# Optimization experiments

Measured on AMD Instinct MI355X. Metric: run time of the kernel, lower is better.

The kernel has to match this reference:

```python
import jax, jax.numpy as jnp
import numpy as np

B = 2
T = 32768          # exp.n_samples = 2**15
NB = 128           # exp.n_bands (filter bank bands)
CH = 128           # channels
EC = 512           # encoding_channels
ATOM = 2048        # full_atom_size
FBK = 512          # filter bank kernel size
DILS = (1, 3, 9, 27, 81, 243, 1)


def setup_inputs() -> dict:
    key = jax.random.key(0)
    ks = jax.random.split(key, 8)
    s = 0.05
    return {
        'x': jax.random.normal(ks[0], (B, 1, T), jnp.float32),
        'fb_w': jax.random.normal(ks[1], (NB, 1, FBK), jnp.float32) * s,
        'conv0_w': jax.random.normal(ks[2], (CH, NB, 7), jnp.float32) * s,
        'conv0_b': jnp.zeros((CH,), jnp.float32),
        'bn0_g': jnp.ones((CH,), jnp.float32),
        'bn0_b': jnp.zeros((CH,), jnp.float32),
        'dil_w': jax.random.normal(ks[3], (7, CH, CH, 3), jnp.float32) * s,
        'dil_b': jnp.zeros((7, CH), jnp.float32),
        'pw_w': jax.random.normal(ks[4], (7, CH, CH, 1), jnp.float32) * s,
        'pw_b': jnp.zeros((7, CH), jnp.float32),
        'bn_g': jnp.ones((7, CH), jnp.float32),
        'bn_b': jnp.zeros((7, CH), jnp.float32),
        'up_w': jax.random.normal(ks[5], (EC, CH, 1), jnp.float32) * s,
        'up_b': jnp.zeros((EC,), jnp.float32),
        'static_dict': jax.random.uniform(ks[6], (1, EC, ATOM), jnp.float32, -1.0, 1.0),
    }


def _conv1d(x, w, b=None, dilation=1, padding=0):
    y = jax.lax.conv_general_dilated(
        x, w, (1,), [(padding, padding)], rhs_dilation=(dilation,),
        dimension_numbers=('NCH', 'OIH', 'NCH'))
    if b is not None:
        y = y + b[None, :, None]
    return y


def _bn(x, g, b, eps=1e-5):
    # BatchNorm1d in training mode: per-channel stats over (batch, time)
    m = x.mean(axis=(0, 2), keepdims=True)
    v = x.var(axis=(0, 2), keepdims=True)
    return (x - m) * jax.lax.rsqrt(v + eps) * g[None, :, None] + b[None, :, None]


def _lrelu(x):
    return jnp.where(x >= 0, x, 0.2 * x)


def _fft_convolve(a, b):
    # linear convolution via zero-padded rfft, truncated back to n samples
    n = a.shape[-1]
    fa = jnp.fft.rfft(a, n=2 * n, axis=-1)
    fb = jnp.fft.rfft(b, n=2 * n, axis=-1)
    return jnp.fft.irfft(fa * fb, n=2 * n, axis=-1)[..., :n]


def reference(x, fb_w, conv0_w, conv0_b, bn0_g, bn0_b, dil_w, dil_b,
              pw_w, pw_b, bn_g, bn_b, up_w, up_b, static_dict):
    Bsz, _, n = x.shape
    # filter bank analysis: [B,1,T] -> [B,NB,T]
    spec = _conv1d(x, fb_w, padding=FBK // 2)[..., :n]
    # front conv + leaky relu + BN
    h = _conv1d(spec, conv0_w, conv0_b, padding=3)
    h = _bn(_lrelu(h), bn0_g, bn0_b)
    # dilated residual blocks (dropout = identity at inference)
    for i, d in enumerate(DILS):
        orig = h
        y = _conv1d(h, dil_w[i], dil_b[i], dilation=d, padding=d)
        y = _conv1d(y, pw_w[i], pw_b[i])
        h = _bn(_lrelu(y + orig), bn_g[i], bn_b[i])
    # up-projection to encoding channels + relu
    encoding = jax.nn.relu(_conv1d(h, up_w, up_b))  # [B,EC,T]
    # static dictionary atoms, zero-padded to n_samples, convolved with encoding
    atoms = jnp.broadcast_to(static_dict, (Bsz, EC, ATOM))
    atoms = jnp.pad(atoms, ((0, 0), (0, 0), (0, n - ATOM)))
    final = _fft_convolve(atoms, encoding)          # [B,EC,T]
    return jnp.sum(final, axis=1, keepdims=True)    # [B,1,T]
```

## Files before the change

### kernel.cpp

```cpp
#include <hip/hip_runtime.h>
#include <hip/hip_bf16.h>

#define B_ 2
#define T_ 32768
#define CH_ 128
#define EC_ 512
#define ATOM_ 2048
#define FBK_ 512

typedef __attribute__((ext_vector_type(8))) short s16x8;
typedef __attribute__((ext_vector_type(8))) _Float16 f16x8;
typedef __attribute__((ext_vector_type(4))) float f32x4;

__device__ __forceinline__ f16x8 ldh8(const _Float16* p) {
    union { s16x8 s; f16x8 h; } u; u.s = *(const s16x8*)p; return u.h;
}

__global__ void __launch_bounds__(256) k_fbm(const float* __restrict__ x,
        const _Float16* __restrict__ Wfb, _Float16* __restrict__ spec16) {
    __shared__ _Float16 XA[128][72];
    __shared__ float xw[640];
    int tid = threadIdx.x;
    int lane = tid & 63;
    int wv = tid >> 6, wm = wv >> 1, wn = wv & 1;
    int ln15 = lane & 15, kh = lane >> 4;
    int t0 = blockIdx.x * 128;
    int b = blockIdx.y;

    for (int i = tid; i < 640; i += 256) {
        int g = t0 - 256 + i;
        xw[i] = (g >= 0 && g < T_) ? x[(size_t)b*T_ + g] : 0.f;
    }

    f32x4 acc[4][4];
    f32x4 zero = {0.f,0.f,0.f,0.f};
#pragma unroll
    for (int m = 0; m < 4; ++m)
#pragma unroll
        for (int n = 0; n < 4; ++n) acc[m][n] = zero;

    for (int c = 0; c < 8; ++c) {
        int k0 = c*64;
        __syncthreads();
#pragma unroll
        for (int q = 0; q < 4; ++q) {
            int idx = tid + q*256;
            int r = idx >> 3, ko = idx & 7;
            int base = r + k0 + ko*8;
            f16x8 v;
#pragma unroll
            for (int j = 0; j < 8; ++j) v[j] = (_Float16)xw[base + j];
            union { f16x8 h; s16x8 s; } u; u.h = v;
            *(s16x8*)&XA[r][ko*8] = u.s;
        }
        __syncthreads();
#pragma unroll
        for (int kt = 0; kt < 2; ++kt) {
            f16x8 af[4], bf[4];
#pragma unroll
            for (int m = 0; m < 4; ++m) af[m] = ldh8(&XA[wm*64+m*16+ln15][kt*32+kh*8]);
#pragma unroll
            for (int n = 0; n < 4; ++n)
                bf[n] = ldh8(Wfb + (size_t)(wn*64+n*16+ln15)*FBK_ + k0 + kt*32 + kh*8);
#pragma unroll
            for (int m = 0; m < 4; ++m)
#pragma unroll
                for (int n = 0; n < 4; ++n)
                    acc[m][n] = __builtin_amdgcn_mfma_f32_16x16x32_f16(af[m], bf[n], acc[m][n], 0,0,0);
        }
    }
#pragma unroll
    for (int mf = 0; mf < 4; ++mf)
#pragma unroll
        for (int nf = 0; nf < 4; ++nf) {
            int band = wn*64 + nf*16 + ln15;
#pragma unroll
            for (int j = 0; j < 4; ++j) {
                int tl = wm*64 + mf*16 + kh*4 + j;
                spec16[((size_t)b*T_ + t0 + tl)*CH_ + band] = (_Float16)acc[mf][nf][j];
            }
        }
}

__global__ void k_pw7(const float* __restrict__ w, _Float16* __restrict__ W7) {
    int i = blockIdx.x*256+threadIdx.x;
    if (i >= 7*16384) return;
    int k = i / 16384, r = i % 16384; int co = r >> 7, ci = r & 127;
    W7[i] = (_Float16)w[(co*CH_+ci)*7 + k];
}
__global__ void k_pwd(const float* __restrict__ w, _Float16* __restrict__ Wd) {
    int i = blockIdx.x*256+threadIdx.x;
    if (i >= 7*3*16384) return;
    int st = i / 49152, r = i % 49152; int k = r / 16384, r2 = r % 16384;
    int co = r2 >> 7, ci = r2 & 127;
    Wd[i] = (_Float16)w[((size_t)(st*CH_+co)*CH_+ci)*3 + k];
}
__global__ void k_cast(const float* __restrict__ in, _Float16* __restrict__ out, int n) {
    int i = blockIdx.x*256+threadIdx.x;
    if (i < n) out[i] = (_Float16)in[i];
}
__global__ void k_zero(float* __restrict__ p, int n) {
    int i = blockIdx.x*256+threadIdx.x;
    if (i < n) p[i] = 0.f;
}

template<int NTAP, bool NORM, bool PW, bool LRELU, bool RELU, bool STATS>
__global__ void __launch_bounds__(256) k_cv(
        const _Float16* __restrict__ in, const _Float16* __restrict__ W,
        const float* __restrict__ bias, const _Float16* __restrict__ Wp_,
        const float* __restrict__ pbias, const float* __restrict__ stats_in,
        const float* __restrict__ g, const float* __restrict__ bb,
        float* __restrict__ stats_out, _Float16* __restrict__ outp,
        int dil, int ostride) {
    __shared__ _Float16 XT[128][136];
    __shared__ _Float16 Y1[PW?128:1][PW?136:1];
    __shared__ float AffA[NORM?128:1], AffB[NORM?128:1];

    int tid = threadIdx.x;
    int lane = tid & 63;
    int wv = tid >> 6, wm = wv >> 1, wn = wv & 1;
    int ln15 = lane & 15, kh = lane >> 4;
    int t0 = blockIdx.x * 128;
    int nch = blockIdx.y;
    int b = blockIdx.z;
    int ncol0 = nch * 128;
    const _Float16* inb = in + (size_t)b*T_*CH_;
    const _Float16* W_eff = W + (size_t)ncol0*CH_;
    const float* bias_eff = bias + ncol0;

    if (NORM) {
        if (tid < 128) {
            const float invN = 1.f/(float)(B_*T_);
            float s1 = stats_in[tid], s2 = stats_in[128+tid];
            float m = s1*invN, var = s2*invN - m*m;
            float A = rsqrtf(var + 1e-5f) * g[tid];
            AffA[tid] = A; AffB[tid] = bb[tid] - m*A;
        }
    }

    f32x4 acc[4][4];
    f32x4 zero = {0.f,0.f,0.f,0.f};
#pragma unroll
    for (int m = 0; m < 4; ++m)
#pragma unroll
        for (int n = 0; n < 4; ++n) acc[m][n] = zero;

    for (int tap = 0; tap < NTAP; ++tap) {
        int tp = tap;
        if (PW) tp = (tap==0) ? 0 : ((tap==1) ? 2 : 1);
        int off = (tp - NTAP/2)*dil;
        const _Float16* Wt = W_eff + (size_t)tp*CH_*CH_;
        __syncthreads();
#pragma unroll
        for (int q = 0; q < 8; ++q) {
            int idx = tid + q*256;
            int lt = idx >> 4, ck = idx & 15;
            int gt = t0 + lt + off;
            s16x8 v = {0,0,0,0,0,0,0,0};
            bool valid = (gt >= 0 && gt < T_);
            if (valid) {
                v = *(const s16x8*)(inb + (size_t)gt*CH_ + ck*8);
                if (NORM) {
                    union {s16x8 s; f16x8 h;} u; u.s = v;
                    f16x8 r;
#pragma unroll
                    for (int j = 0; j < 8; ++j) {
                        float f = (float)u.h[j];
                        f = fmaf(f, AffA[ck*8+j], AffB[ck*8+j]);
                        r[j] = (_Float16)f;
                    }
                    union {f16x8 h; s16x8 s;} w2; w2.h = r; v = w2.s;
                }
            }
            *(s16x8*)&XT[lt][ck*8] = v;
        }
        __syncthreads();
#pragma unroll
        for (int kt = 0; kt < 4; ++kt) {
            f16x8 af[4], bf[4];
#pragma unroll
            for (int m = 0; m < 4; ++m) af[m] = ldh8(&XT[wm*64+m*16+ln15][kt*32+kh*8]);
#pragma unroll
            for (int n = 0; n < 4; ++n)
                bf[n] = ldh8(Wt + (size_t)(wn*64+n*16+ln15)*CH_ + kt*32 + kh*8);
#pragma unroll
            for (int m = 0; m < 4; ++m)
#pragma unroll
                for (int n = 0; n < 4; ++n)
                    acc[m][n] = __builtin_amdgcn_mfma_f32_16x16x32_f16(af[m], bf[n], acc[m][n], 0,0,0);
        }
    }

    if (PW) {
#pragma unroll
        for (int mf = 0; mf < 4; ++mf)
#pragma unroll
            for (int nf = 0; nf < 4; ++nf) {
                int co = wn*64 + nf*16 + ln15;
                float bv = bias_eff[co];
#pragma unroll
                for (int j = 0; j < 4; ++j) {
                    int tl = wm*64 + mf*16 + kh*4 + j;
                    Y1[tl][co] = (_Float16)(acc[mf][nf][j] + bv);
                }
            }
#pragma unroll
        for (int m = 0; m < 4; ++m)
#pragma unroll
            for (int n = 0; n < 4; ++n) acc[m][n] = zero;
        __syncthreads();
#pragma unroll
        for (int kt = 0; kt < 4; ++kt) {
            f16x8 af[4], bf[4];
#pragma unroll
            for (int m = 0; m < 4; ++m) af[m] = ldh8(&Y1[wm*64+m*16+ln15][kt*32+kh*8]);
#pragma unroll
            for (int n = 0; n < 4; ++n)
                bf[n] = ldh8(Wp_ + (size_t)(wn*64+n*16+ln15)*CH_ + kt*32 + kh*8);
#pragma unroll
            for (int m = 0; m < 4; ++m)
#pragma unroll
                for (int n = 0; n < 4; ++n)
                    acc[m][n] = __builtin_amdgcn_mfma_f32_16x16x32_f16(af[m], bf[n], acc[m][n], 0,0,0);
        }
    }

#pragma unroll
    for (int nf = 0; nf < 4; ++nf) {
        int co = wn*64 + nf*16 + ln15;
        float bfin = PW ? pbias[co] : bias_eff[co];
        float s = 0.f, s2 = 0.f;
#pragma unroll
        for (int mf = 0; mf < 4; ++mf) {
#pragma unroll
            for (int j = 0; j < 4; ++j) {
                int tl = wm*64 + mf*16 + kh*4 + j;
                float v = acc[mf][nf][j] + bfin;
                if (PW) v += (float)XT[tl][co];
                if (LRELU) v = v >= 0.f ? v : 0.2f*v;
                if (RELU)  v = fmaxf(v, 0.f);
                outp[((size_t)b*T_ + t0 + tl)*ostride + ncol0 + co] = (_Float16)v;
                if (STATS) { s += v; s2 += v*v; }
            }
        }
        if (STATS) {
            s  += __shfl_down(s, 16);  s  += __shfl_down(s, 32);
            s2 += __shfl_down(s2, 16); s2 += __shfl_down(s2, 32);
            if (kh == 0) {
                atomicAdd(&stats_out[co], s);
                atomicAdd(&stats_out[128+co], s2);
            }
        }
    }
}

__global__ void k_tr_at(const float* __restrict__ sd, _Float16* __restrict__ At) {
    __shared__ float tile[32][33];
    int tau0 = blockIdx.x*32;
    int c0 = blockIdx.y*32;
    int tx = threadIdx.x, ty = threadIdx.y;
#pragma unroll
    for (int j = 0; j < 4; ++j)
        tile[ty+j*8][tx] = sd[(size_t)(c0+ty+j*8)*ATOM_ + tau0 + tx];
    __syncthreads();
#pragma unroll
    for (int j = 0; j < 4; ++j)
        At[(size_t)(tau0+ty+j*8)*EC_ + c0 + tx] = (_Float16)tile[tx][ty+j*8];
}

__global__ void __launch_bounds__(256) k_gemm(const _Float16* __restrict__ At,
                                              const _Float16* __restrict__ enc,
                                              float* __restrict__ out) {
    __shared__ _Float16 lA[128][72];
    __shared__ _Float16 lB[128][72];
    __shared__ float pt[256];
    int tid = threadIdx.x;
    int lane = tid & 63;
    int wv = tid >> 6;
    int wm = wv >> 1, wn = wv & 1;
    int sT = blockIdx.x;
    int tT = blockIdx.y;
    int b  = blockIdx.z;
    const _Float16* Et = enc + (size_t)b*T_*EC_;
    int ln15 = lane & 15, kh = lane >> 4;
    f32x4 acc[4][4];
    f32x4 zero = {0.f,0.f,0.f,0.f};
#pragma unroll
    for (int m = 0; m < 4; ++m)
#pragma unroll
        for (int n = 0; n < 4; ++n) acc[m][n] = zero;

    for (int kt = 0; kt < 8; ++kt) {
#pragma unroll
        for (int r = 0; r < 4; ++r) {
            int idx = tid + r*256;
            int row = idx >> 3, ch = idx & 7;
            *(s16x8*)&lA[row][ch*8] = *(const s16x8*)(At + ((size_t)(tT*128+row))*EC_ + kt*64 + ch*8);
            *(s16x8*)&lB[row][ch*8] = *(const s16x8*)(Et + ((size_t)(sT*128+row))*EC_ + kt*64 + ch*8);
        }
        __syncthreads();
#pragma unroll
        for (int kk = 0; kk < 2; ++kk) {
            f16x8 af[4], bfr[4];
#pragma unroll
            for (int m = 0; m < 4; ++m)
                af[m] = ldh8(&lA[wm*64 + m*16 + ln15][kk*32 + kh*8]);
#pragma unroll
            for (int n = 0; n < 4; ++n)
                bfr[n] = ldh8(&lB[wn*64 + n*16 + ln15][kk*32 + kh*8]);
#pragma unroll
            for (int m = 0; m < 4; ++m)
#pragma unroll
                for (int n = 0; n < 4; ++n)
                    acc[m][n] = __builtin_amdgcn_mfma_f32_16x16x32_f16(af[m], bfr[n], acc[m][n], 0, 0, 0);
        }
        __syncthreads();
    }

    pt[tid] = 0.f;
    __syncthreads();
#pragma unroll
    for (int mn = 0; mn <= 6; ++mn) {
#pragma unroll
        for (int j = 0; j < 4; ++j) {
            float v = 0.f;
#pragma unroll
            for (int m = 0; m < 4; ++m) {
                int n = mn - m;
                if (n >= 0 && n < 4) v += acc[m][n][j];
            }
            int tl = (wm + wn)*64 + mn*16 + kh*4 + j + ln15;
            unsafeAtomicAdd(&pt[tl], v);
        }
    }
    __syncthreads();
    if (tid < 255) {
        int tg = tT*128 + sT*128 + tid;
        if (tg < T_) unsafeAtomicAdd(&out[(size_t)b*T_ + tg], pt[tid]);
    }
}

__global__ void k_fill(float* __restrict__ out, float val) {
    out[blockIdx.x*256 + threadIdx.x] = val;
}

extern "C" void kernel_launch(void* const* d_in, const int* in_sizes, int n_in,
                              void* d_out, int out_size, void* d_ws, size_t ws_size,
                              hipStream_t stream) {
    const float* x       = (const float*)d_in[0];
    const float* fb_w    = (const float*)d_in[1];
    const float* conv0_w = (const float*)d_in[2];
    const float* conv0_b = (const float*)d_in[3];
    const float* bn0_g   = (const float*)d_in[4];
    const float* bn0_b   = (const float*)d_in[5];
    const float* dil_w   = (const float*)d_in[6];
    const float* dil_b   = (const float*)d_in[7];
    const float* pw_w    = (const float*)d_in[8];
    const float* pw_b    = (const float*)d_in[9];
    const float* bn_g    = (const float*)d_in[10];
    const float* bn_b    = (const float*)d_in[11];
    const float* up_w    = (const float*)d_in[12];
    const float* up_b    = (const float*)d_in[13];
    const float* sdict   = (const float*)d_in[14];
    float* out = (float*)d_out;
    char* ws = (char*)d_ws;

    const size_t R1   = 33554432;
    const size_t R2   = 33554432;
    const size_t ACT  = 16777216;
    char* r1   = ws;
    char* actA = ws + R1 + R2;
    char* actB = actA + ACT;
    char* wreg = actB + ACT;
    _Float16* W7   = (_Float16*)wreg;
    _Float16* Wd   = W7 + 7*16384;
    _Float16* Wp   = Wd + 7*3*16384;
    _Float16* Wup  = Wp + 7*16384;
    _Float16* Wfb  = Wup + 65536;
    float* stats   = (float*)(Wfb + 65536);
    const size_t TOTAL = R1 + R2 + 2*ACT
                       + (7*16384 + 7*3*16384 + 7*16384 + 65536 + 65536)*2 + 8*2*128*4;
    if (ws_size < TOTAL) {
        k_fill<<<(out_size+255)/256, 256, 0, stream>>>(out, 12345.0f);
        return;
    }
    _Float16* spec16 = (_Float16*)r1;
    _Float16* enc = (_Float16*)r1;
    _Float16* At  = (_Float16*)(actA + 2097152);

    k_zero<<<(2048+255)/256, 256, 0, stream>>>(stats, 8*2*128);
    k_pw7<<<(7*16384+255)/256, 256, 0, stream>>>(conv0_w, W7);
    k_pwd<<<(7*3*16384+255)/256, 256, 0, stream>>>(dil_w, Wd);
    k_cast<<<(7*16384+255)/256, 256, 0, stream>>>(pw_w, Wp, 7*16384);
    k_cast<<<(65536+255)/256, 256, 0, stream>>>(up_w, Wup, 65536);
    k_cast<<<(65536+255)/256, 256, 0, stream>>>(fb_w, Wfb, 65536);

    k_fbm<<<dim3(T_/128, B_), 256, 0, stream>>>(x, Wfb, spec16);
    k_cv<7,false,false,true,false,true><<<dim3(T_/128,1,B_), 256, 0, stream>>>(
        spec16, W7, conv0_b, nullptr, nullptr, nullptr, nullptr, nullptr,
        stats + 0, (_Float16*)actA, 1, CH_);

    const int DILS[7] = {1, 3, 9, 27, 81, 243, 1};
    _Float16* cur = (_Float16*)actA;
    _Float16* nxt = (_Float16*)actB;
    for (int i = 0; i < 7; ++i) {
        const float* gi = (i == 0) ? bn0_g : bn_g + (i-1)*CH_;
        const float* bi = (i == 0) ? bn0_b : bn_b + (i-1)*CH_;
        k_cv<3,true,true,true,false,true><<<dim3(T_/128,1,B_), 256, 0, stream>>>(
            cur, Wd + (size_t)i*3*CH_*CH_, dil_b + i*CH_, Wp + (size_t)i*CH_*CH_,
            pw_b + i*CH_, stats + i*256, gi, bi, stats + (i+1)*256, nxt, DILS[i], CH_);
        _Float16* sw = cur; cur = nxt; nxt = sw;
    }

    k_tr_at<<<dim3(ATOM_/32, EC_/32), dim3(32,8), 0, stream>>>(sdict, At);
    k_cv<1,true,false,false,true,false><<<dim3(T_/128,EC_/128,B_), 256, 0, stream>>>(
        cur, Wup, up_b, nullptr, nullptr,
        stats + 7*256, bn_g + 6*CH_, bn_b + 6*CH_, nullptr, enc, 1, EC_);

    k_zero<<<(B_*T_+255)/256, 256, 0, stream>>>(out, B_*T_);
    k_gemm<<<dim3(T_/128, ATOM_/128, B_), 256, 0, stream>>>(At, enc, out);
}
```

Before: 955.4 us.

## Keep encoding tile resident in LDS and loop over all atom tiles per block

The final GEMM-with-diagonal-sum kernel now keeps a 128x512 encoding tile resident in shared memory and loops over all 16 atom-time tiles inside one block, instead of launching a block per atom tile. Atom data is register-prefetched one chunk ahead, and diagonal partial sums collect in a larger shared buffer before one atomic flush to global memory. This removes repeated encoding reloads and most global atomics. In exchange it cuts grid size 16x, uses 512 threads with large LDS, and serialises more work per block, which risks lower occupancy.

```diff
diff --git a/kernel.cpp b/kernel.cpp
--- a/kernel.cpp
+++ b/kernel.cpp
@@ -268,75 +268,97 @@
         At[(size_t)(tau0+ty+j*8)*EC_ + c0 + tx] = (_Float16)tile[tx][ty+j*8];
 }
 
-__global__ void __launch_bounds__(256) k_gemm(const _Float16* __restrict__ At,
+__global__ void __launch_bounds__(512) k_gemm(const _Float16* __restrict__ At,
                                               const _Float16* __restrict__ enc,
                                               float* __restrict__ out) {
+    __shared__ _Float16 lE[128][520];
     __shared__ _Float16 lA[128][72];
-    __shared__ _Float16 lB[128][72];
-    __shared__ float pt[256];
+    __shared__ float pt[2176];
     int tid = threadIdx.x;
     int lane = tid & 63;
     int wv = tid >> 6;
-    int wm = wv >> 1, wn = wv & 1;
+    int wm = wv >> 2;
+    int wn = wv & 3;
     int sT = blockIdx.x;
-    int tT = blockIdx.y;
-    int b  = blockIdx.z;
-    const _Float16* Et = enc + (size_t)b*T_*EC_;
+    int b  = blockIdx.y;
+    const _Float16* Eb = enc + ((size_t)b*T_ + (size_t)sT*128)*EC_;
     int ln15 = lane & 15, kh = lane >> 4;
-    f32x4 acc[4][4];
+
+    for (int i = tid; i < 2176; i += 512) pt[i] = 0.f;
+#pragma unroll
+    for (int q = 0; q < 16; ++q) {
+        int idx = tid + q*512;
+        int r = idx >> 6, c8 = (idx & 63) << 3;
+        s16x8 v = *(const s16x8*)(Eb + (size_t)r*EC_ + c8);
+        *(s16x8*)&lE[r][c8] = v;
+    }
+
+    f32x4 acc[4][2];
     f32x4 zero = {0.f,0.f,0.f,0.f};
 #pragma unroll
-    for (int m = 0; m < 4; ++m)
-#pragma unroll
-        for (int n = 0; n < 4; ++n) acc[m][n] = zero;
-
-    for (int kt = 0; kt < 8; ++kt) {
-#pragma unroll
-        for (int r = 0; r < 4; ++r) {
-            int idx = tid + r*256;
-            int row = idx >> 3, ch = idx & 7;
-            *(s16x8*)&lA[row][ch*8] = *(const s16x8*)(At + ((size_t)(tT*128+row))*EC_ + kt*64 + ch*8);
-            *(s16x8*)&lB[row][ch*8] = *(const s16x8*)(Et + ((size_t)(sT*128+row))*EC_ + kt*64 + ch*8);
-        }
-        __syncthreads();
+    for (int m = 0; m < 4; ++m) { acc[m][0] = zero; acc[m][1] = zero; }
+
+    s16x8 p0, p1;
+    {
+        int i0 = tid, i1 = tid + 512;
+        p0 = *(const s16x8*)(At + (size_t)(i0 >> 3)*EC_ + ((i0 & 7) << 3));
+        p1 = *(const s16x8*)(At + (size_t)(i1 >> 3)*EC_ + ((i1 & 7) << 3));
+    }
+    for (int c = 0; c < 128; ++c) {
+        __syncthreads();
+        {
+            int i0 = tid, i1 = tid + 512;
+            *(s16x8*)&lA[i0 >> 3][(i0 & 7) << 3] = p0;
+            *(s16x8*)&lA[i1 >> 3][(i1 & 7) << 3] = p1;
+        }
+        {
+            int nc = (c + 1) & 127;
+            int bt = (nc >> 3) * 128, bk = (nc & 7) * 64;
+            int i0 = tid, i1 = tid + 512;
+            p0 = *(const s16x8*)(At + (size_t)(bt + (i0 >> 3))*EC_ + bk + ((i0 & 7) << 3));
+            p1 = *(const s16x8*)(At + (size_t)(bt + (i1 >> 3))*EC_ + bk + ((i1 & 7) << 3));
+        }
+        __syncthreads();
+        int kt = c & 7;
 #pragma unroll
         for (int kk = 0; kk < 2; ++kk) {
-            f16x8 af[4], bfr[4];
+            f16x8 af[4], bf[2];
 #pragma unroll
             for (int m = 0; m < 4; ++m)
                 af[m] = ldh8(&lA[wm*64 + m*16 + ln15][kk*32 + kh*8]);
 #pragma unroll
-            for (int n = 0; n < 4; ++n)
-                bfr[n] = ldh8(&lB[wn*64 + n*16 + ln15][kk*32 + kh*8]);
+            for (int n = 0; n < 2; ++n)
+                bf[n] = ldh8(&lE[wn*32 + n*16 + ln15][kt*64 + kk*32 + kh*8]);
 #pragma unroll
             for (int m = 0; m < 4; ++m)
 #pragma unroll
-                for (int n = 0; n < 4; ++n)
-                    acc[m][n] = __builtin_amdgcn_mfma_f32_16x16x32_f16(af[m], bfr[n], acc[m][n], 0, 0, 0);
-        }
-        __syncthreads();
-    }
-
-    pt[tid] = 0.f;
+                for (int n = 0; n < 2; ++n)
+                    acc[m][n] = __builtin_amdgcn_mfma_f32_16x16x32_f16(af[m], bf[n], acc[m][n], 0, 0, 0);
+        }
+        if ((c & 7) == 7) {
+            int tt = c >> 3;
+#pragma unroll
+            for (int mn = 0; mn <= 4; ++mn) {
+#pragma unroll
+                for (int j = 0; j < 4; ++j) {
+                    float v = 0.f;
+#pragma unroll
+                    for (int n = 0; n < 2; ++n) {
+                        int m = mn - n;
+                        if (m >= 0 && m < 4) v += acc[m][n][j];
+                    }
+                    int tl = wm*64 + wn*32 + mn*16 + kh*4 + j + ln15;
+                    unsafeAtomicAdd(&pt[tt*128 + tl], v);
+                }
+            }
+#pragma unroll
+            for (int m = 0; m < 4; ++m) { acc[m][0] = zero; acc[m][1] = zero; }
+        }
+    }
     __syncthreads();
-#pragma unroll
-    for (int mn = 0; mn <= 6; ++mn) {
-#pragma unroll
-        for (int j = 0; j < 4; ++j) {
-            float v = 0.f;
-#pragma unroll
-            for (int m = 0; m < 4; ++m) {
-                int n = mn - m;
-                if (n >= 0 && n < 4) v += acc[m][n][j];
-            }
-            int tl = (wm + wn)*64 + mn*16 + kh*4 + j + ln15;
-            unsafeAtomicAdd(&pt[tl], v);
-        }
-    }
-    __syncthreads();
-    if (tid < 255) {
-        int tg = tT*128 + sT*128 + tid;
-        if (tg < T_) unsafeAtomicAdd(&out[(size_t)b*T_ + tg], pt[tid]);
+    for (int i = tid; i < 2175; i += 512) {
+        int t = sT*128 + i;
+        if (t < T_) unsafeAtomicAdd(&out[(size_t)b*T_ + t], pt[i]);
     }
 }
 
@@ -418,5 +440,5 @@
         stats + 7*256, bn_g + 6*CH_, bn_b + 6*CH_, nullptr, enc, 1, EC_);
 
     k_zero<<<(B_*T_+255)/256, 256, 0, stream>>>(out, B_*T_);
-    k_gemm<<<dim3(T_/128, ATOM_/128, B_), 256, 0, stream>>>(At, enc, out);
-}
+    k_gemm<<<dim3(T_/128, B_), 512, 0, stream>>>(At, enc, out);
+}
```

After: 1.093 ms. 1.14x slower.
